# Kernel optimization log

Measured on AMD Instinct MI355X. Metric: run time of the kernel, lower is better.

Reference implementation:

```python
import jax, jax.numpy as jnp
import numpy as np

N_GENE, N_DRUG = 20000, 3000
D_GENE, D_DRUG = 1024, 512
H = [256, 128]
E_GG, E_DD, E_DT = 600000, 120000, 150000
P_DROP = 0.2


def _dropout(x, key):
    # F.dropout(p=0.2, training=True) with a fixed key for determinism
    keep = jax.random.bernoulli(key, 1.0 - P_DROP, x.shape)
    return jnp.where(keep, x / (1.0 - P_DROP), 0.0).astype(x.dtype)


def _gcn_norm(x, W, b, edge_index, n):
    src, dst = edge_index[0], edge_index[1]
    loops = jnp.arange(n, dtype=src.dtype)
    src = jnp.concatenate([src, loops])
    dst = jnp.concatenate([dst, loops])
    deg = jax.ops.segment_sum(jnp.ones(src.shape, x.dtype), dst, num_segments=n)
    dinv = jax.lax.rsqrt(deg)  # deg >= 1 thanks to self loops
    xw = x @ W  # [n_src, out]
    msg = xw[src] * (dinv[src] * dinv[dst])[:, None]  # [E+n, out]
    return jax.ops.segment_sum(msg, dst, num_segments=n) + b


def _gcn_plain(x, W, b, edge_index, n_dst):
    # PyG GCNConv(add_self_loops=False, normalize=False): A X W + b (bipartite scatter)
    xw = x @ W
    return jax.ops.segment_sum(xw[edge_index[0]], edge_index[1], num_segments=n_dst) + b


def _l2norm(x):
    # F.normalize(dim=1, p=2), eps=1e-12
    n = jnp.linalg.norm(x, axis=1, keepdims=True)
    return x / jnp.maximum(n, 1e-12)


def setup_inputs() -> dict:
    key = jax.random.key(0)
    ks = jax.random.split(key, 32)
    inp = {}
    inp["gene_feat"] = jax.random.normal(ks[0], (N_GENE, D_GENE), jnp.float32)
    inp["drug_feat"] = jax.random.normal(ks[1], (N_DRUG, D_DRUG), jnp.float32)
    inp["ei_gg"] = jax.random.randint(ks[2], (2, E_GG), 0, N_GENE)
    inp["ei_dd"] = jax.random.randint(ks[3], (2, E_DD), 0, N_DRUG)
    # drug_target: messages from drug (src row) to gene (dst row)
    inp["ei_dt"] = jnp.stack([jax.random.randint(ks[4], (E_DT,), 0, N_DRUG),
                               jax.random.randint(ks[5], (E_DT,), 0, N_GENE)])
    # target_drug: messages from gene (src row) to drug (dst row)
    inp["ei_td"] = jnp.stack([jax.random.randint(ks[6], (E_DT,), 0, N_GENE),
                               jax.random.randint(ks[7], (E_DT,), 0, N_DRUG)])
    dims_in = {"gg": D_GENE, "dd": D_DRUG, "dt": D_DRUG, "td": D_GENE}
    i = 8
    for l, h in enumerate(H):
        for et in ["gg", "dd", "dt", "td"]:
            din = dims_in[et] if l == 0 else H[l - 1]
            s = float(1.0 / np.sqrt(din))
            inp[f"W{l}_{et}"] = jax.random.uniform(ks[i], (din, h), jnp.float32, -s, s)
            i += 1
            inp[f"b{l}_{et}"] = jnp.zeros((h,), jnp.float32)
    return inp


def reference(gene_feat, drug_feat, ei_gg, ei_dd, ei_dt, ei_td,
              W0_gg, b0_gg, W0_dd, b0_dd, W0_dt, b0_dt, W0_td, b0_td,
              W1_gg, b1_gg, W1_dd, b1_dd, W1_dt, b1_dt, W1_td, b1_td):
    dk = jax.random.split(jax.random.key(42), 8)
    layers = [
        ((W0_gg, b0_gg), (W0_dd, b0_dd), (W0_dt, b0_dt), (W0_td, b0_td)),
        ((W1_gg, b1_gg), (W1_dd, b1_dd), (W1_dt, b1_dt), (W1_td, b1_td)),
    ]
    xg, xd = gene_feat, drug_feat
    k = 0
    for (Wgg, bgg), (Wdd, bdd), (Wdt, bdt), (Wtd, btd) in layers:
        gg = jax.nn.relu(_gcn_norm(_dropout(xg, dk[k + 0]), Wgg, bgg, ei_gg, N_GENE))
        dd = jax.nn.relu(_gcn_norm(_dropout(xd, dk[k + 1]), Wdd, bdd, ei_dd, N_DRUG))
        dt = jax.nn.relu(_gcn_plain(_dropout(xd, dk[k + 2]), Wdt, bdt, ei_dt, N_GENE))
        td = jax.nn.relu(_gcn_plain(_dropout(xg, dk[k + 3]), Wtd, btd, ei_td, N_DRUG))
        # per-edge-type L2 normalize, then sum contributions per node type
        xg = _l2norm(gg) + _l2norm(dt)
        xd = _l2norm(dd) + _l2norm(td)
        k += 4
    # concat node-type outputs: genes first, drugs second -> [N_GENE+N_DRUG, H[-1]]
    return jnp.concatenate([xg, xd], axis=0)
```

## Files before the change

### kernel.cpp

```cpp
#include <hip/hip_runtime.h>
#include <stdint.h>

#define N_GENE 20000
#define N_DRUG 3000
#define D_GENE 1024
#define D_DRUG 512
#define H0 256
#define H1 128
#define E_GG 600000
#define E_DD 120000
#define E_DT 150000

typedef __attribute__((ext_vector_type(8))) short bf16x8;
typedef __attribute__((ext_vector_type(4))) float f32x4;

__host__ __device__ inline uint32_t rotl32(uint32_t x, int d) {
#ifdef __HIP_DEVICE_COMPILE__
    return __builtin_amdgcn_alignbit(x, x, 32 - d);
#else
    return (x << d) | (x >> (32 - d));
#endif
}

__host__ __device__ inline void tf2x32(uint32_t k0, uint32_t k1, uint32_t x0, uint32_t x1,
                                       uint32_t& o0, uint32_t& o1) {
    uint32_t ks2 = k0 ^ k1 ^ 0x1BD11BDAu;
    x0 += k0; x1 += k1;
#define TFR(r) { x0 += x1; x1 = rotl32(x1, r); x1 ^= x0; }
    TFR(13) TFR(15) TFR(26) TFR(6)
    x0 += k1; x1 += ks2 + 1u;
    TFR(17) TFR(29) TFR(16) TFR(24)
    x0 += ks2; x1 += k0 + 2u;
    TFR(13) TFR(15) TFR(26) TFR(6)
    x0 += k0; x1 += k1 + 3u;
    TFR(17) TFR(29) TFR(16) TFR(24)
    x0 += k1; x1 += ks2 + 4u;
    TFR(13) TFR(15) TFR(26) TFR(6)
    x0 += ks2; x1 += k0 + 5u;
#undef TFR
    o0 = x0; o1 = x1;
}

__device__ inline short f2bf(float f) {
    uint32_t u = __float_as_uint(f);
    uint32_t r = (u + 0x7FFFu + ((u >> 16) & 1u)) >> 16;
    return (short)r;
}
__device__ inline float bf_lo(uint32_t u) { return __uint_as_float(u << 16); }
__device__ inline float bf_hi(uint32_t u) { return __uint_as_float(u & 0xFFFF0000u); }

__device__ inline uint4 maskpack8(float4 xa, float4 xb, unsigned local, uint32_t k0, uint32_t k1) {
    float xv[8] = {xa.x, xa.y, xa.z, xa.w, xb.x, xb.y, xb.z, xb.w};
    union { short s[8]; uint4 u; } st;
#pragma unroll
    for (int i = 0; i < 8; i++) {
        uint32_t a, b;
        tf2x32(k0, k1, 0u, local + (unsigned)i, a, b);
        uint32_t bits = a ^ b;
        st.s[i] = ((bits >> 9) < 6710887u) ? f2bf(xv[i] * 1.25f) : (short)0;
    }
    return st.u;
}

#define CUM_E0 600000u
#define CUM_E1 720000u
#define CUM_E2 870000u
#define CUM_E3 1020000u

__global__ void count4_kernel(const int* __restrict__ gg, const int* __restrict__ dd,
                              const int* __restrict__ dt, const int* __restrict__ td,
                              int* __restrict__ cnt) {
    unsigned e = blockIdx.x * 256u + threadIdx.x;
    if (e >= CUM_E3) return;
    const int* dsts; unsigned base, noff;
    if (e >= CUM_E2)      { dsts = td + E_DT; base = CUM_E2; noff = 43000; }
    else if (e >= CUM_E1) { dsts = dt + E_DT; base = CUM_E1; noff = 23000; }
    else if (e >= CUM_E0) { dsts = dd + E_DD; base = CUM_E0; noff = 20000; }
    else                  { dsts = gg + E_GG; base = 0;      noff = 0; }
    atomicAdd(&cnt[noff + dsts[e - base]], 1);
}

__global__ __launch_bounds__(1024) void scan_p1(const int* __restrict__ cnt,
                                                int* __restrict__ tmp, int* __restrict__ bsum) {
    __shared__ int buf[1024];
    int tid = threadIdx.x;
    int i = blockIdx.x * 1024 + tid;
    int v = (i < 46000) ? cnt[i] : 0;
    buf[tid] = v;
    __syncthreads();
    for (int off = 1; off < 1024; off <<= 1) {
        int t = (tid >= off) ? buf[tid - off] : 0;
        __syncthreads();
        buf[tid] += t;
        __syncthreads();
    }
    if (i < 46000) tmp[i] = buf[tid];
    if (tid == 1023) bsum[blockIdx.x] = buf[1023];
}

__global__ void scan_p2(int* __restrict__ bsum) {
    int lane = threadIdx.x;
    int v = (lane < 45) ? bsum[lane] : 0;
    int orig = v;
    for (int off = 1; off < 64; off <<= 1) {
        int t = __shfl_up(v, off, 64);
        if (lane >= off) v += t;
    }
    if (lane < 45) bsum[lane] = v - orig;
}

__global__ __launch_bounds__(1024) void scan_p3(const int* __restrict__ cnt,
                                                const int* __restrict__ tmp,
                                                const int* __restrict__ bsum,
                                                int* __restrict__ rpall, int* __restrict__ pos,
                                                float* __restrict__ dinv_g,
                                                float* __restrict__ dinv_d) {
    int i = blockIdx.x * 1024 + threadIdx.x;
    if (i < 46000) {
        int g = tmp[i] - cnt[i] + bsum[blockIdx.x];
        rpall[i] = g;
        pos[i] = g;
        if (i < 20000) dinv_g[i] = 1.0f / sqrtf((float)cnt[i] + 1.0f);
        else if (i < 23000) dinv_d[i - 20000] = 1.0f / sqrtf((float)cnt[i] + 1.0f);
    }
    if (i == 0) rpall[46000] = (int)CUM_E3;
}

struct CastT4P {
    unsigned c0, c1, c2, c3;
    int lgK0, lgK1, lgK2, lgK3;
    int N;
};
__global__ __launch_bounds__(256) void fillcastT_kernel(
    const int* __restrict__ gg, const int* __restrict__ dd,
    const int* __restrict__ dt, const int* __restrict__ td,
    int* __restrict__ pos, int* __restrict__ col,
    const float* __restrict__ W0, const float* __restrict__ W1,
    const float* __restrict__ W2, const float* __restrict__ W3,
    short* __restrict__ Wt, CastT4P P, int fillBlocks) {
    int bx = blockIdx.x;
    if (bx < fillBlocks) {
        unsigned e = (unsigned)bx * 256u + threadIdx.x;
        if (e >= CUM_E3) return;
        const int* ei; unsigned base, noff; int E;
        if (e >= CUM_E2)      { ei = td; base = CUM_E2; noff = 43000; E = E_DT; }
        else if (e >= CUM_E1) { ei = dt; base = CUM_E1; noff = 23000; E = E_DT; }
        else if (e >= CUM_E0) { ei = dd; base = CUM_E0; noff = 20000; E = E_DD; }
        else                  { ei = gg; base = 0;      noff = 0;     E = E_GG; }
        unsigned local = e - base;
        int src = ei[local], dst = ei[E + local];
        int p = atomicAdd(&pos[noff + dst], 1);
        col[p] = src;
        return;
    }
    unsigned idx = (unsigned)(bx - fillBlocks) * 256u + threadIdx.x;
    if (idx >= P.c3) return;
    unsigned base; const float* W; int lgK;
    if (idx >= P.c2)      { base = P.c2; W = W3; lgK = P.lgK3; }
    else if (idx >= P.c1) { base = P.c1; W = W2; lgK = P.lgK2; }
    else if (idx >= P.c0) { base = P.c0; W = W1; lgK = P.lgK1; }
    else                  { base = 0u;   W = W0; lgK = P.lgK0; }
    unsigned local = idx - base;
    unsigned n = local >> lgK, k = local & ((1u << lgK) - 1u);
    Wt[idx] = f2bf(W[(size_t)k * P.N + n]);
}

__global__ __launch_bounds__(256) void castT4_kernel(
    const float* __restrict__ W0, const float* __restrict__ W1,
    const float* __restrict__ W2, const float* __restrict__ W3,
    short* __restrict__ Wt, CastT4P P) {
    unsigned idx = blockIdx.x * 256u + threadIdx.x;
    if (idx >= P.c3) return;
    unsigned base; const float* W; int lgK;
    if (idx >= P.c2)      { base = P.c2; W = W3; lgK = P.lgK3; }
    else if (idx >= P.c1) { base = P.c1; W = W2; lgK = P.lgK2; }
    else if (idx >= P.c0) { base = P.c0; W = W1; lgK = P.lgK1; }
    else                  { base = 0u;   W = W0; lgK = P.lgK0; }
    unsigned local = idx - base;
    unsigned n = local >> lgK, k = local & ((1u << lgK) - 1u);
    Wt[idx] = f2bf(W[(size_t)k * P.N + n]);
}

struct GDescF { const float* X; unsigned boff, coff; const float* rs; int M, K, mb0; uint32_t k0, k1; };
#define LDP 72
template <int BN>
__global__ __launch_bounds__(512) void gemm4f_kernel(
    const short* __restrict__ Wb, short* __restrict__ Cb,
    GDescF d0, GDescF d1, GDescF d2, GDescF d3) {
    constexpr int WN = BN / 4;
    constexpr int NF = WN / 16;
    constexpr int SB = BN / 64;
    __shared__ short As[64 * LDP];
    __shared__ short Bs[BN * LDP];
    GDescF d;
    int bx = blockIdx.x;
    if (bx >= d3.mb0) d = d3;
    else if (bx >= d2.mb0) d = d2;
    else if (bx >= d1.mb0) d = d1;
    else d = d0;
    bx -= d.mb0;
    const int M = d.M, K = d.K;
    const short* Bt = Wb + d.boff;
    short* C = Cb + d.coff;

    int tid = threadIdx.x;
    int lane = tid & 63, w = tid >> 6;
    int m = lane & 15, kb = lane >> 4;
    int m0w = (w >> 2) * 32, n0w = (w & 3) * WN;
    int gm = bx * 64;

    int ar = tid >> 3, ac = (tid & 7) * 8;
    int agr = min(gm + ar, M - 1);
    const float* pax = d.X + (size_t)agr * K + ac;
    unsigned alocal = (unsigned)agr * (unsigned)K + (unsigned)ac;

    int brr[SB], bcc[SB];
    const short* pb[SB];
#pragma unroll
    for (int i = 0; i < SB; i++) {
        int flat = tid + 512 * i;
        brr[i] = flat >> 3; bcc[i] = (flat & 7) * 8;
        pb[i] = Bt + (size_t)brr[i] * K + bcc[i];
    }

    f32x4 acc[2][NF];
#pragma unroll
    for (int i = 0; i < 2; i++)
#pragma unroll
        for (int j = 0; j < NF; j++) acc[i][j] = (f32x4){0.f, 0.f, 0.f, 0.f};

    float4 xa = *(const float4*)pax;
    float4 xb = *(const float4*)(pax + 4);
    uint4 rb[SB];
#pragma unroll
    for (int i = 0; i < SB; i++) rb[i] = *(const uint4*)pb[i];
    uint4 a8 = maskpack8(xa, xb, alocal, d.k0, d.k1);

    int nt = K >> 6;
    for (int t = 0; t < nt; ++t) {
        __syncthreads();
        *(uint4*)&As[ar * LDP + ac] = a8;
#pragma unroll
        for (int i = 0; i < SB; i++) *(uint4*)&Bs[brr[i] * LDP + bcc[i]] = rb[i];
        __syncthreads();
        if (t + 1 < nt) {
            int kt = (t + 1) << 6;
            xa = *(const float4*)(pax + kt);
            xb = *(const float4*)(pax + kt + 4);
#pragma unroll
            for (int i = 0; i < SB; i++) rb[i] = *(const uint4*)(pb[i] + kt);
            a8 = maskpack8(xa, xb, alocal + (unsigned)kt, d.k0, d.k1);
        }
#pragma unroll
        for (int ks = 0; ks < 2; ++ks) {
            bf16x8 a0 = *(const bf16x8*)&As[(m0w + m) * LDP + ks * 32 + kb * 8];
            bf16x8 a1 = *(const bf16x8*)&As[(m0w + 16 + m) * LDP + ks * 32 + kb * 8];
#pragma unroll
            for (int nf = 0; nf < NF; nf++) {
                bf16x8 bf = *(const bf16x8*)&Bs[(n0w + nf * 16 + m) * LDP + ks * 32 + kb * 8];
                acc[0][nf] = __builtin_amdgcn_mfma_f32_16x16x32_bf16(a0, bf, acc[0][nf], 0, 0, 0);
                acc[1][nf] = __builtin_amdgcn_mfma_f32_16x16x32_bf16(a1, bf, acc[1][nf], 0, 0, 0);
            }
        }
    }
#pragma unroll
    for (int mf = 0; mf < 2; ++mf)
#pragma unroll
        for (int j = 0; j < 4; ++j) {
            int r = gm + m0w + mf * 16 + kb * 4 + j;
            if (r < M) {
                float s = d.rs ? d.rs[r] : 1.0f;
#pragma unroll
                for (int nf = 0; nf < NF; ++nf)
                    C[(size_t)r * BN + n0w + nf * 16 + m] = f2bf(acc[mf][nf][j] * s);
            }
        }
}

template <int F>
__global__ __launch_bounds__(256) void agg2_kernel(
    const short* __restrict__ XWa, const int* __restrict__ rpa,
    const float* __restrict__ dinv, const float* __restrict__ ba,
    const short* __restrict__ XWb2, const int* __restrict__ rpb,
    const float* __restrict__ bb, const int* __restrict__ col,
    float* __restrict__ out, int n_dst) {
    const int h = 64 * F;
    int lane = threadIdx.x & 63;
    int row = blockIdx.x * 4 + (threadIdx.x >> 6);
    if (row >= n_dst) return;
    int c0 = lane * F;
    float acc[F], va[F];

#pragma unroll
    for (int i = 0; i < F; i++) acc[i] = 0.f;
    {
        if constexpr (F == 4) {
            uint2 u = *(const uint2*)(XWa + (size_t)row * h + c0);
            acc[0] += bf_lo(u.x); acc[1] += bf_hi(u.x);
            acc[2] += bf_lo(u.y); acc[3] += bf_hi(u.y);
        } else {
            uint32_t u = *(const uint32_t*)(XWa + (size_t)row * h + c0);
            acc[0] += bf_lo(u); acc[1] += bf_hi(u);
        }
        int s0 = rpa[row], s1 = rpa[row + 1];
        int p = s0;
        for (; p + 8 <= s1; p += 8) {
            int c[8];
#pragma unroll
            for (int i = 0; i < 8; i++) c[i] = col[p + i];
            if constexpr (F == 4) {
                uint2 g[8];
#pragma unroll
                for (int i = 0; i < 8; i++) g[i] = *(const uint2*)(XWa + (size_t)c[i] * h + c0);
#pragma unroll
                for (int i = 0; i < 8; i++) {
                    acc[0] += bf_lo(g[i].x); acc[1] += bf_hi(g[i].x);
                    acc[2] += bf_lo(g[i].y); acc[3] += bf_hi(g[i].y);
                }
            } else {
                uint32_t g[8];
#pragma unroll
                for (int i = 0; i < 8; i++) g[i] = *(const uint32_t*)(XWa + (size_t)c[i] * h + c0);
#pragma unroll
                for (int i = 0; i < 8; i++) { acc[0] += bf_lo(g[i]); acc[1] += bf_hi(g[i]); }
            }
        }
        for (; p < s1; p++) {
            int s = col[p];
            if constexpr (F == 4) {
                uint2 u = *(const uint2*)(XWa + (size_t)s * h + c0);
                acc[0] += bf_lo(u.x); acc[1] += bf_hi(u.x);
                acc[2] += bf_lo(u.y); acc[3] += bf_hi(u.y);
            } else {
                uint32_t u = *(const uint32_t*)(XWa + (size_t)s * h + c0);
                acc[0] += bf_lo(u); acc[1] += bf_hi(u);
            }
        }
    }
    float mul = dinv[row];
    float ssa = 0.f;
#pragma unroll
    for (int i = 0; i < F; i++) {
        float v = fmaxf(acc[i] * mul + ba[c0 + i], 0.f);
        va[i] = v;
        ssa += v * v;
    }

#pragma unroll
    for (int i = 0; i < F; i++) acc[i] = 0.f;
    {
        int s0 = rpb[row], s1 = rpb[row + 1];
        int p = s0;
        for (; p + 8 <= s1; p += 8) {
            int c[8];
#pragma unroll
            for (int i = 0; i < 8; i++) c[i] = col[p + i];
            if constexpr (F == 4) {
                uint2 g[8];
#pragma unroll
                for (int i = 0; i < 8; i++) g[i] = *(const uint2*)(XWb2 + (size_t)c[i] * h + c0);
#pragma unroll
                for (int i = 0; i < 8; i++) {
                    acc[0] += bf_lo(g[i].x); acc[1] += bf_hi(g[i].x);
                    acc[2] += bf_lo(g[i].y); acc[3] += bf_hi(g[i].y);
                }
            } else {
                uint32_t g[8];
#pragma unroll
                for (int i = 0; i < 8; i++) g[i] = *(const uint32_t*)(XWb2 + (size_t)c[i] * h + c0);
#pragma unroll
                for (int i = 0; i < 8; i++) { acc[0] += bf_lo(g[i]); acc[1] += bf_hi(g[i]); }
            }
        }
        for (; p < s1; p++) {
            int s = col[p];
            if constexpr (F == 4) {
                uint2 u = *(const uint2*)(XWb2 + (size_t)s * h + c0);
                acc[0] += bf_lo(u.x); acc[1] += bf_hi(u.x);
                acc[2] += bf_lo(u.y); acc[3] += bf_hi(u.y);
            } else {
                uint32_t u = *(const uint32_t*)(XWb2 + (size_t)s * h + c0);
                acc[0] += bf_lo(u); acc[1] += bf_hi(u);
            }
        }
    }
    float ssb = 0.f;
#pragma unroll
    for (int i = 0; i < F; i++) {
        float v = fmaxf(acc[i] + bb[c0 + i], 0.f);
        acc[i] = v;
        ssb += v * v;
    }

#pragma unroll
    for (int off = 32; off >= 1; off >>= 1) {
        ssa += __shfl_xor(ssa, off, 64);
        ssb += __shfl_xor(ssb, off, 64);
    }
    float sa = 1.0f / fmaxf(sqrtf(ssa), 1e-12f);
    float sb = 1.0f / fmaxf(sqrtf(ssb), 1e-12f);
    float* orow = out + (size_t)row * h + c0;
    if constexpr (F == 4) {
        *(float4*)orow = make_float4(va[0] * sa + acc[0] * sb, va[1] * sa + acc[1] * sb,
                                     va[2] * sa + acc[2] * sb, va[3] * sa + acc[3] * sb);
    } else {
        *(float2*)orow = make_float2(va[0] * sa + acc[0] * sb, va[1] * sa + acc[1] * sb);
    }
}

extern "C" void kernel_launch(void* const* d_in, const int* in_sizes, int n_in,
                              void* d_out, int out_size, void* d_ws, size_t ws_size,
                              hipStream_t stream) {
    const float* gene = (const float*)d_in[0];
    const float* drug = (const float*)d_in[1];
    const int* ei_gg = (const int*)d_in[2];
    const int* ei_dd = (const int*)d_in[3];
    const int* ei_dt = (const int*)d_in[4];
    const int* ei_td = (const int*)d_in[5];
    const float* W0gg = (const float*)d_in[6];  const float* b0gg = (const float*)d_in[7];
    const float* W0dd = (const float*)d_in[8];  const float* b0dd = (const float*)d_in[9];
    const float* W0dt = (const float*)d_in[10]; const float* b0dt = (const float*)d_in[11];
    const float* W0td = (const float*)d_in[12]; const float* b0td = (const float*)d_in[13];
    const float* W1gg = (const float*)d_in[14]; const float* b1gg = (const float*)d_in[15];
    const float* W1dd = (const float*)d_in[16]; const float* b1dd = (const float*)d_in[17];
    const float* W1dt = (const float*)d_in[18]; const float* b1dt = (const float*)d_in[19];
    const float* W1td = (const float*)d_in[20]; const float* b1td = (const float*)d_in[21];

    uint32_t dk[8][2];
    for (uint32_t i = 0; i < 8; i++) tf2x32(0u, 42u, 0u, i, dk[i][0], dk[i][1]);

    char* p = (char*)d_ws;
    auto take = [&](size_t bytes) -> void* {
        void* r = (void*)p;
        p += (bytes + 255) & ~(size_t)255;
        return r;
    };
    short* XW   = (short*)take(sizeof(short) * 11776000ULL);
    short* Wt   = (short*)take(sizeof(short) * 786432ULL);
    float* xg1  = (float*)take(sizeof(float) * (size_t)N_GENE * H0);
    float* xd1  = (float*)take(sizeof(float) * (size_t)N_DRUG * H0);
    float* dinv_g = (float*)take(sizeof(float) * N_GENE);
    float* dinv_d = (float*)take(sizeof(float) * N_DRUG);
    int* cnt   = (int*)take(4 * 46000);
    int* tmp   = (int*)take(4 * 46000);
    int* bsum  = (int*)take(4 * 64);
    int* pos   = (int*)take(4 * 46000);
    int* rpall = (int*)take(4 * 46001);
    int* col   = (int*)take(4 * 1020000);

    const int* rp_gg = rpall;
    const int* rp_dd = rpall + 20000;
    const int* rp_dt = rpall + 23000;
    const int* rp_td = rpall + 43000;

    hipMemsetAsync(cnt, 0, 4 * 46000, stream);
    count4_kernel<<<(1020000 + 255) / 256, 256, 0, stream>>>(ei_gg, ei_dd, ei_dt, ei_td, cnt);
    scan_p1<<<45, 1024, 0, stream>>>(cnt, tmp, bsum);
    scan_p2<<<1, 64, 0, stream>>>(bsum);
    scan_p3<<<45, 1024, 0, stream>>>(cnt, tmp, bsum, rpall, pos, dinv_g, dinv_d);
    CastT4P tp0 = {262144u, 524288u, 655360u, 786432u, 10, 10, 9, 9, H0};
    int fillBlocks = (1020000 + 255) / 256;
    fillcastT_kernel<<<fillBlocks + (786432 + 255) / 256, 256, 0, stream>>>(
        ei_gg, ei_dd, ei_dt, ei_td, pos, col,
        W0gg, W0td, W0dd, W0dt, Wt, tp0, fillBlocks);

    {
        GDescF g0 = {gene, 0u,      0u,        dinv_g,  N_GENE, 1024, 0,   dk[0][0], dk[0][1]};
        GDescF g1 = {gene, 262144u, 5120000u,  nullptr, N_GENE, 1024, 313, dk[3][0], dk[3][1]};
        GDescF g2 = {drug, 524288u, 10240000u, dinv_d,  N_DRUG, 512,  626, dk[1][0], dk[1][1]};
        GDescF g3 = {drug, 655360u, 11008000u, nullptr, N_DRUG, 512,  673, dk[2][0], dk[2][1]};
        gemm4f_kernel<256><<<720, 512, 0, stream>>>(Wt, XW, g0, g1, g2, g3);
        agg2_kernel<4><<<(N_GENE + 3) / 4, 256, 0, stream>>>(
            XW, rp_gg, dinv_g, b0gg, XW + 11008000, rp_dt, b0dt, col, xg1, N_GENE);
        agg2_kernel<4><<<(N_DRUG + 3) / 4, 256, 0, stream>>>(
            XW + 10240000, rp_dd, dinv_d, b0dd, XW + 5120000, rp_td, b0td, col, xd1, N_DRUG);
    }

    {
        CastT4P tp1 = {32768u, 65536u, 98304u, 131072u, 8, 8, 8, 8, H1};
        castT4_kernel<<<(131072 + 255) / 256, 256, 0, stream>>>(W1gg, W1td, W1dd, W1dt, Wt, tp1);
        GDescF g0 = {xg1, 0u,     0u,        dinv_g,  N_GENE, 256, 0,   dk[4][0], dk[4][1]};
        GDescF g1 = {xg1, 32768u, 5120000u,  nullptr, N_GENE, 256, 313, dk[7][0], dk[7][1]};
        GDescF g2 = {xd1, 65536u, 10240000u, dinv_d,  N_DRUG, 256, 626, dk[5][0], dk[5][1]};
        GDescF g3 = {xd1, 98304u, 11008000u, nullptr, N_DRUG, 256, 673, dk[6][0], dk[6][1]};
        gemm4f_kernel<128><<<720, 512, 0, stream>>>(Wt, XW, g0, g1, g2, g3);
        float* og = (float*)d_out;
        float* od = og + (size_t)N_GENE * H1;
        agg2_kernel<2><<<(N_GENE + 3) / 4, 256, 0, stream>>>(
            XW, rp_gg, dinv_g, b1gg, XW + 11008000, rp_dt, b1dt, col, og, N_GENE);
        agg2_kernel<2><<<(N_DRUG + 3) / 4, 256, 0, stream>>>(
            XW + 10240000, rp_dd, dinv_d, b1dd, XW + 5120000, rp_td, b1td, col, od, N_DRUG);
    }
}
```

Before: 477.7 us.

## Halve GEMM M-tile to 32 rows, split N across eight waves, fold dropout scale into epilogue

The fused dropout+GEMM kernel now uses 32-row A tiles with each of the 8 waves owning a distinct N slice, roughly doubling the grid to 1438 blocks. Each thread generates 4 dropout masks per K-step instead of 8, spreading the Threefry RNG work over more blocks. Launch bounds now request 4 blocks per SM. The 1.25 dropout scale moves from the per-element pack to the output epilogue multiply. This trades more B-tile reloads per output row (each block reloads the full weight tile for half as many rows) for more parallelism and less per-thread RNG latency.

New measurement: 522.2 us. 9.3% more time.

```diff
diff --git a/kernel.cpp b/kernel.cpp
--- a/kernel.cpp
+++ b/kernel.cpp
@@ -49,15 +49,15 @@
 __device__ inline float bf_lo(uint32_t u) { return __uint_as_float(u << 16); }
 __device__ inline float bf_hi(uint32_t u) { return __uint_as_float(u & 0xFFFF0000u); }
 
-__device__ inline uint4 maskpack8(float4 xa, float4 xb, unsigned local, uint32_t k0, uint32_t k1) {
-    float xv[8] = {xa.x, xa.y, xa.z, xa.w, xb.x, xb.y, xb.z, xb.w};
-    union { short s[8]; uint4 u; } st;
-#pragma unroll
-    for (int i = 0; i < 8; i++) {
+__device__ inline uint2 maskpack4(float4 x, unsigned local, uint32_t k0, uint32_t k1) {
+    float xv[4] = {x.x, x.y, x.z, x.w};
+    union { short s[4]; uint2 u; } st;
+#pragma unroll
+    for (int i = 0; i < 4; i++) {
         uint32_t a, b;
         tf2x32(k0, k1, 0u, local + (unsigned)i, a, b);
         uint32_t bits = a ^ b;
-        st.s[i] = ((bits >> 9) < 6710887u) ? f2bf(xv[i] * 1.25f) : (short)0;
+        st.s[i] = ((bits >> 9) < 6710887u) ? f2bf(xv[i]) : (short)0;
     }
     return st.u;
 }
@@ -184,13 +184,13 @@
 struct GDescF { const float* X; unsigned boff, coff; const float* rs; int M, K, mb0; uint32_t k0, k1; };
 #define LDP 72
 template <int BN>
-__global__ __launch_bounds__(512) void gemm4f_kernel(
+__global__ __launch_bounds__(512, 4) void gemmf_kernel(
     const short* __restrict__ Wb, short* __restrict__ Cb,
     GDescF d0, GDescF d1, GDescF d2, GDescF d3) {
-    constexpr int WN = BN / 4;
+    constexpr int WN = BN / 8;
     constexpr int NF = WN / 16;
     constexpr int SB = BN / 64;
-    __shared__ short As[64 * LDP];
+    __shared__ short As[32 * LDP];
     __shared__ short Bs[BN * LDP];
     GDescF d;
     int bx = blockIdx.x;
@@ -206,10 +206,10 @@
     int tid = threadIdx.x;
     int lane = tid & 63, w = tid >> 6;
     int m = lane & 15, kb = lane >> 4;
-    int m0w = (w >> 2) * 32, n0w = (w & 3) * WN;
-    int gm = bx * 64;
-
-    int ar = tid >> 3, ac = (tid & 7) * 8;
+    int n0w = w * WN;
+    int gm = bx * 32;
+
+    int ar = tid >> 4, ac = (tid & 15) * 4;
     int agr = min(gm + ar, M - 1);
     const float* pax = d.X + (size_t)agr * K + ac;
     unsigned alocal = (unsigned)agr * (unsigned)K + (unsigned)ac;
@@ -230,31 +230,29 @@
         for (int j = 0; j < NF; j++) acc[i][j] = (f32x4){0.f, 0.f, 0.f, 0.f};
 
     float4 xa = *(const float4*)pax;
-    float4 xb = *(const float4*)(pax + 4);
     uint4 rb[SB];
 #pragma unroll
     for (int i = 0; i < SB; i++) rb[i] = *(const uint4*)pb[i];
-    uint4 a8 = maskpack8(xa, xb, alocal, d.k0, d.k1);
+    uint2 a4 = maskpack4(xa, alocal, d.k0, d.k1);
 
     int nt = K >> 6;
     for (int t = 0; t < nt; ++t) {
         __syncthreads();
-        *(uint4*)&As[ar * LDP + ac] = a8;
+        *(uint2*)&As[ar * LDP + ac] = a4;
 #pragma unroll
         for (int i = 0; i < SB; i++) *(uint4*)&Bs[brr[i] * LDP + bcc[i]] = rb[i];
         __syncthreads();
         if (t + 1 < nt) {
             int kt = (t + 1) << 6;
             xa = *(const float4*)(pax + kt);
-            xb = *(const float4*)(pax + kt + 4);
 #pragma unroll
             for (int i = 0; i < SB; i++) rb[i] = *(const uint4*)(pb[i] + kt);
-            a8 = maskpack8(xa, xb, alocal + (unsigned)kt, d.k0, d.k1);
+            a4 = maskpack4(xa, alocal + (unsigned)kt, d.k0, d.k1);
         }
 #pragma unroll
         for (int ks = 0; ks < 2; ++ks) {
-            bf16x8 a0 = *(const bf16x8*)&As[(m0w + m) * LDP + ks * 32 + kb * 8];
-            bf16x8 a1 = *(const bf16x8*)&As[(m0w + 16 + m) * LDP + ks * 32 + kb * 8];
+            bf16x8 a0 = *(const bf16x8*)&As[m * LDP + ks * 32 + kb * 8];
+            bf16x8 a1 = *(const bf16x8*)&As[(16 + m) * LDP + ks * 32 + kb * 8];
 #pragma unroll
             for (int nf = 0; nf < NF; nf++) {
                 bf16x8 bf = *(const bf16x8*)&Bs[(n0w + nf * 16 + m) * LDP + ks * 32 + kb * 8];
@@ -267,9 +265,9 @@
     for (int mf = 0; mf < 2; ++mf)
 #pragma unroll
         for (int j = 0; j < 4; ++j) {
-            int r = gm + m0w + mf * 16 + kb * 4 + j;
+            int r = gm + mf * 16 + kb * 4 + j;
             if (r < M) {
-                float s = d.rs ? d.rs[r] : 1.0f;
+                float s = (d.rs ? d.rs[r] : 1.0f) * 1.25f;
 #pragma unroll
                 for (int nf = 0; nf < NF; ++nf)
                     C[(size_t)r * BN + n0w + nf * 16 + m] = f2bf(acc[mf][nf][j] * s);
@@ -465,11 +463,11 @@
         W0gg, W0td, W0dd, W0dt, Wt, tp0, fillBlocks);
 
     {
-        GDescF g0 = {gene, 0u,      0u,        dinv_g,  N_GENE, 1024, 0,   dk[0][0], dk[0][1]};
-        GDescF g1 = {gene, 262144u, 5120000u,  nullptr, N_GENE, 1024, 313, dk[3][0], dk[3][1]};
-        GDescF g2 = {drug, 524288u, 10240000u, dinv_d,  N_DRUG, 512,  626, dk[1][0], dk[1][1]};
-        GDescF g3 = {drug, 655360u, 11008000u, nullptr, N_DRUG, 512,  673, dk[2][0], dk[2][1]};
-        gemm4f_kernel<256><<<720, 512, 0, stream>>>(Wt, XW, g0, g1, g2, g3);
+        GDescF g0 = {gene, 0u,      0u,        dinv_g,  N_GENE, 1024, 0,    dk[0][0], dk[0][1]};
+        GDescF g1 = {gene, 262144u, 5120000u,  nullptr, N_GENE, 1024, 625,  dk[3][0], dk[3][1]};
+        GDescF g2 = {drug, 524288u, 10240000u, dinv_d,  N_DRUG, 512,  1250, dk[1][0], dk[1][1]};
+        GDescF g3 = {drug, 655360u, 11008000u, nullptr, N_DRUG, 512,  1344, dk[2][0], dk[2][1]};
+        gemmf_kernel<256><<<1438, 512, 0, stream>>>(Wt, XW, g0, g1, g2, g3);
         agg2_kernel<4><<<(N_GENE + 3) / 4, 256, 0, stream>>>(
             XW, rp_gg, dinv_g, b0gg, XW + 11008000, rp_dt, b0dt, col, xg1, N_GENE);
         agg2_kernel<4><<<(N_DRUG + 3) / 4, 256, 0, stream>>>(
@@ -479,11 +477,11 @@
     {
         CastT4P tp1 = {32768u, 65536u, 98304u, 131072u, 8, 8, 8, 8, H1};
         castT4_kernel<<<(131072 + 255) / 256, 256, 0, stream>>>(W1gg, W1td, W1dd, W1dt, Wt, tp1);
-        GDescF g0 = {xg1, 0u,     0u,        dinv_g,  N_GENE, 256, 0,   dk[4][0], dk[4][1]};
-        GDescF g1 = {xg1, 32768u, 5120000u,  nullptr, N_GENE, 256, 313, dk[7][0], dk[7][1]};
-        GDescF g2 = {xd1, 65536u, 10240000u, dinv_d,  N_DRUG, 256, 626, dk[5][0], dk[5][1]};
-        GDescF g3 = {xd1, 98304u, 11008000u, nullptr, N_DRUG, 256, 673, dk[6][0], dk[6][1]};
-        gemm4f_kernel<128><<<720, 512, 0, stream>>>(Wt, XW, g0, g1, g2, g3);
+        GDescF g0 = {xg1, 0u,     0u,        dinv_g,  N_GENE, 256, 0,    dk[4][0], dk[4][1]};
+        GDescF g1 = {xg1, 32768u, 5120000u,  nullptr, N_GENE, 256, 625,  dk[7][0], dk[7][1]};
+        GDescF g2 = {xd1, 65536u, 10240000u, dinv_d,  N_DRUG, 256, 1250, dk[5][0], dk[5][1]};
+        GDescF g3 = {xd1, 98304u, 11008000u, nullptr, N_DRUG, 256, 1344, dk[6][0], dk[6][1]};
+        gemmf_kernel<128><<<1438, 512, 0, stream>>>(Wt, XW, g0, g1, g2, g3);
         float* og = (float*)d_out;
         float* od = og + (size_t)N_GENE * H1;
         agg2_kernel<2><<<(N_GENE + 3) / 4, 256, 0, stream>>>(
```
